# Performance work log

Hardware: AMD Instinct MI355X
Metric: run time of the kernel (lower is better)

The kernel has to match this reference:

```python
import jax, jax.numpy as jnp
import numpy as np
import math

B, S, DIM = 2, 2048, 2048
H, KV = 32, 8
HD = DIM // H          # 64
REP = H // KV          # 4
NEG = -1e9


def setup_inputs() -> dict:
    key = jax.random.key(0)
    ks = jax.random.split(key, 8)
    x = jax.random.normal(ks[0], (B, S, DIM), dtype=jnp.float32)
    # RoPE frequencies: theta = 10000^{-2i/d}, angles = pos * theta
    inv_freq = 1.0 / (10000.0 ** (jnp.arange(0, HD, 2, dtype=jnp.float32) / HD))  # [HD/2]
    angles = jnp.arange(S, dtype=jnp.float32)[:, None] * inv_freq[None, :]        # [S, HD/2]
    freqs_cos = jnp.cos(angles)
    freqs_sin = jnp.sin(angles)
    # additive causal mask [1,1,S,S]
    causal = jnp.tril(jnp.ones((S, S), dtype=bool))
    mask = jnp.where(causal, 0.0, NEG).astype(jnp.float32)[None, None]
    sc = 1.0 / math.sqrt(DIM)
    wq = jax.random.normal(ks[1], (DIM, H * HD), dtype=jnp.float32) * sc
    wk = jax.random.normal(ks[2], (DIM, KV * HD), dtype=jnp.float32) * sc
    wv = jax.random.normal(ks[3], (DIM, KV * HD), dtype=jnp.float32) * sc
    wo = jax.random.normal(ks[4], (H * HD, DIM), dtype=jnp.float32) * sc
    return {"x": x, "freqs_cos": freqs_cos, "freqs_sin": freqs_sin,
            "mask": mask, "wq": wq, "wk": wk, "wv": wv, "wo": wo}


def _rope(t, cos, sin):
    # t: [B,S,nh,HD]; interleaved (even, odd) pairs == view_as_complex layout
    te, to = t[..., 0::2], t[..., 1::2]
    c = cos[None, :, None, :]  # [1,S,1,HD/2]
    s = sin[None, :, None, :]
    oe = te * c - to * s
    oo = te * s + to * c
    return jnp.stack([oe, oo], axis=-1).reshape(t.shape)


def reference(x, freqs_cos, freqs_sin, mask, wq, wk, wv, wo):
    b, s, _ = x.shape
    q = (x @ wq).reshape(b, s, H, HD)
    k = (x @ wk).reshape(b, s, KV, HD)
    v = (x @ wv).reshape(b, s, KV, HD)
    q = _rope(q, freqs_cos, freqs_sin)
    k = _rope(k, freqs_cos, freqs_sin)
    # GQA without materializing repeat_interleave: group q heads by kv head
    # repeat_interleave maps query head h -> kv head h // REP
    qg = q.transpose(0, 2, 1, 3).reshape(b, KV, REP, s, HD)  # [B,KV,REP,S,HD]
    kg = k.transpose(0, 2, 1, 3)                              # [B,KV,S,HD]
    vg = v.transpose(0, 2, 1, 3)
    scores = jnp.einsum('bgrqd,bgkd->bgrqk', qg, kg) / math.sqrt(HD)
    scores = scores + mask[:, :, None]                        # [1,1,1,S,S] broadcast
    attn = jax.nn.softmax(scores, axis=-1)
    out = jnp.einsum('bgrqk,bgkd->bgrqd', attn, vg)           # [B,KV,REP,S,HD]
    out = out.reshape(b, H, s, HD).transpose(0, 2, 1, 3).reshape(b, s, H * HD)
    return out @ wo
```

## Files before the change

### kernel.cpp

```cpp
#include <hip/hip_runtime.h>
#include <hip/hip_bf16.h>

#define B_ 2
#define S_ 2048
#define DIM_ 2048
#define H_ 32
#define KV_ 8
#define HD_ 64

typedef __bf16 bf16x8 __attribute__((ext_vector_type(8)));
typedef __bf16 bf16x4 __attribute__((ext_vector_type(4)));
typedef float f32x4 __attribute__((ext_vector_type(4)));
typedef float f32x16 __attribute__((ext_vector_type(16)));
typedef unsigned u32x2 __attribute__((ext_vector_type(2)));

#define GLOAD16(gp, lp) __builtin_amdgcn_global_load_lds( \
    (const __attribute__((address_space(1))) void*)(gp),  \
    (__attribute__((address_space(3))) void*)(lp), 16, 0, 0)

__global__ __launch_bounds__(256) void cast_f32_bf16_v4(const float* __restrict__ in,
                                                        __bf16* __restrict__ out, int n4) {
    int i = blockIdx.x * 256 + threadIdx.x;
    if (i >= n4) return;
    float4 v = ((const float4*)in)[i];
    bf16x4 o;
    o[0] = (__bf16)v.x; o[1] = (__bf16)v.y; o[2] = (__bf16)v.z; o[3] = (__bf16)v.w;
    ((bf16x4*)out)[i] = o;
}

__global__ __launch_bounds__(256) void transpose_all_t(const float* __restrict__ wq,
                                                       const float* __restrict__ wk,
                                                       const float* __restrict__ wv,
                                                       const float* __restrict__ wo,
                                                       __bf16* __restrict__ wqkv_t,
                                                       __bf16* __restrict__ wo_t) {
    __shared__ float t[32][33];
    const int bk = blockIdx.x * 32, bn = blockIdx.y * 32;
    const int tx = threadIdx.x & 31, ty = threadIdx.x >> 5;
    const float* W; __bf16* Wt; int N, src;
    if (blockIdx.z == 0) {
        Wt = wqkv_t;
        if (bn < 2048)      { W = wq; N = 2048; src = bn; }
        else if (bn < 2560) { W = wk; N = 512;  src = bn - 2048; }
        else                { W = wv; N = 512;  src = bn - 2560; }
    } else {
        if (bn >= 2048) return;
        Wt = wo_t; W = wo; N = 2048; src = bn;
    }
#pragma unroll
    for (int i = 0; i < 4; i++)
        t[ty * 4 + i][tx] = W[(size_t)(bk + ty * 4 + i) * N + src + tx];
    __syncthreads();
#pragma unroll
    for (int i = 0; i < 4; i++)
        Wt[(size_t)(bn + ty * 4 + i) * 2048 + bk + tx] = (__bf16)t[tx][ty * 4 + i];
}

__global__ __launch_bounds__(512, 2)
void gemm256_qkv(const __bf16* __restrict__ A, const __bf16* __restrict__ Bt,
                 __bf16* __restrict__ q_bf, __bf16* __restrict__ k_bf,
                 __bf16* __restrict__ vt_bf,
                 const float* __restrict__ fc, const float* __restrict__ fs) {
    __shared__ __align__(16) char smem[131072];
    char* lA = smem;
    char* lB = smem + 65536;
    const int K = DIM_;
    const int tid = threadIdx.x, lane = tid & 63, wid = tid >> 6;
    const int wr2 = wid >> 2, wc2 = wid & 3;
    const int fr = lane & 15, fg = lane >> 4;
    const long i0 = (long)blockIdx.x * 256;
    const long j0 = (long)blockIdx.y * 256;

    const int r0 = tid >> 3;
    const int cc = ((tid & 7) ^ (r0 & 7)) * 8;
    const __bf16* pA = A + (i0 + r0) * (long)K + cc;
    const __bf16* pB = Bt + (j0 + r0) * (long)K + cc;
    const int NT = K >> 6;

    f32x4 acc[8][4] = {};

#define STGA(h, kt, buf) do { \
    GLOAD16(pA + (long)((h) * 128) * K + (kt) * 64,      lA + (buf) * 32768 + (h) * 16384 + tid * 16); \
    GLOAD16(pA + (long)((h) * 128 + 64) * K + (kt) * 64, lA + (buf) * 32768 + (h) * 16384 + 8192 + tid * 16); } while (0)
#define STGB(h, kt, buf) do { \
    GLOAD16(pB + (long)((h) * 128) * K + (kt) * 64,      lB + (buf) * 32768 + (h) * 16384 + tid * 16); \
    GLOAD16(pB + (long)((h) * 128 + 64) * K + (kt) * 64, lB + (buf) * 32768 + (h) * 16384 + 8192 + tid * 16); } while (0)

    STGA(0, 0, 0); STGB(0, 0, 0); STGB(1, 0, 0); STGA(1, 0, 0);

    for (int kt = 0; kt < NT; ++kt) {
        const int cur = kt & 1, nxt = cur ^ 1;
        const bool nl = (kt + 1 < NT);
        const char* cA = lA + cur * 32768;
        const char* cB = lB + cur * 32768;
        bf16x8 af[4], bfv[4];

        auto rdA = [&](int mf, int ks) -> bf16x8 {
            int row = wr2 * 128 + mf * 16 + fr;
            return *(const bf16x8*)(cA + row * 128 + (((ks << 2) | fg) ^ (row & 7)) * 16);
        };
        auto rdB = [&](int nf, int ks) -> bf16x8 {
            int row = wc2 * 64 + nf * 16 + fr;
            return *(const bf16x8*)(cB + row * 128 + (((ks << 2) | fg) ^ (row & 7)) * 16);
        };

        if (nl) { STGA(0, kt + 1, nxt); STGB(0, kt + 1, nxt); }
        if (nl) asm volatile("s_waitcnt vmcnt(4)" ::: "memory");
        else    asm volatile("s_waitcnt vmcnt(0)" ::: "memory");
        __builtin_amdgcn_s_barrier();
        asm volatile("" ::: "memory");
#pragma unroll
        for (int nf = 0; nf < 4; nf++) bfv[nf] = rdB(nf, 0);
#pragma unroll
        for (int mf = 0; mf < 4; mf++) af[mf] = rdA(mf, 0);
        __builtin_amdgcn_s_setprio(1);
#pragma unroll
        for (int mf = 0; mf < 4; mf++)
#pragma unroll
            for (int nf = 0; nf < 4; nf++)
                acc[mf][nf] = __builtin_amdgcn_mfma_f32_16x16x32_bf16(af[mf], bfv[nf], acc[mf][nf], 0, 0, 0);
        __builtin_amdgcn_s_setprio(0);
        __builtin_amdgcn_s_barrier();

#pragma unroll
        for (int mf = 0; mf < 4; mf++) af[mf] = rdA(4 + mf, 0);
        if (nl) { STGB(1, kt + 1, nxt); STGA(1, kt + 1, nxt); }
        __builtin_amdgcn_s_barrier();
        __builtin_amdgcn_s_setprio(1);
#pragma unroll
        for (int mf = 0; mf < 4; mf++)
#pragma unroll
            for (int nf = 0; nf < 4; nf++)
                acc[4 + mf][nf] = __builtin_amdgcn_mfma_f32_16x16x32_bf16(af[mf], bfv[nf], acc[4 + mf][nf], 0, 0, 0);
        __builtin_amdgcn_s_setprio(0);
        __builtin_amdgcn_s_barrier();

#pragma unroll
        for (int nf = 0; nf < 4; nf++) bfv[nf] = rdB(nf, 1);
#pragma unroll
        for (int mf = 0; mf < 4; mf++) af[mf] = rdA(mf, 1);
        __builtin_amdgcn_s_barrier();
        __builtin_amdgcn_s_setprio(1);
#pragma unroll
        for (int mf = 0; mf < 4; mf++)
#pragma unroll
            for (int nf = 0; nf < 4; nf++)
                acc[mf][nf] = __builtin_amdgcn_mfma_f32_16x16x32_bf16(af[mf], bfv[nf], acc[mf][nf], 0, 0, 0);
        __builtin_amdgcn_s_setprio(0);
        __builtin_amdgcn_s_barrier();

#pragma unroll
        for (int mf = 0; mf < 4; mf++) af[mf] = rdA(4 + mf, 1);
        __builtin_amdgcn_s_barrier();
        __builtin_amdgcn_s_setprio(1);
#pragma unroll
        for (int mf = 0; mf < 4; mf++)
#pragma unroll
            for (int nf = 0; nf < 4; nf++)
                acc[4 + mf][nf] = __builtin_amdgcn_mfma_f32_16x16x32_bf16(af[mf], bfv[nf], acc[4 + mf][nf], 0, 0, 0);
        __builtin_amdgcn_s_setprio(0);
        __builtin_amdgcn_s_barrier();
    }
#undef STGA
#undef STGB

    const long col0 = j0 + wc2 * 64;
    if (j0 < 2048) {
#pragma unroll
        for (int mf = 0; mf < 8; mf++)
#pragma unroll
            for (int nf = 0; nf < 4; nf++)
#pragma unroll
                for (int j = 0; j < 4; j++) {
                    long row = i0 + wr2 * 128 + mf * 16 + fg * 4 + j;
                    q_bf[row * 2048 + col0 + nf * 16 + fr] = (__bf16)acc[mf][nf][j];
                }
    } else if (j0 < 2560) {
#pragma unroll
        for (int mf = 0; mf < 8; mf++)
#pragma unroll
            for (int nf = 0; nf < 4; nf++) {
                const int kd = (int)(col0 + nf * 16 + fr - 2048);
                const int i_ = (kd & 63) >> 1;
                const float sgn = (fr & 1) ? 1.0f : -1.0f;
#pragma unroll
                for (int j = 0; j < 4; j++) {
                    long row = i0 + wr2 * 128 + mf * 16 + fg * 4 + j;
                    int s = (int)(row & (S_ - 1));
                    float cv = fc[s * 32 + i_], sv = fs[s * 32 + i_];
                    float v = acc[mf][nf][j];
                    float p = __shfl_xor(v, 1, 64);
                    k_bf[row * 512 + kd] = (__bf16)(v * cv + sgn * sv * p);
                }
            }
    } else {
#pragma unroll
        for (int mf = 0; mf < 8; mf++)
#pragma unroll
            for (int nf = 0; nf < 4; nf++) {
                const int vd = (int)(col0 + nf * 16 + fr - 2560);
                long row0 = i0 + wr2 * 128 + mf * 16 + fg * 4;
                int b = (int)(row0 >> 11);
                int s = (int)(row0 & (S_ - 1));
                bf16x4 pk;
#pragma unroll
                for (int j = 0; j < 4; j++) pk[j] = (__bf16)acc[mf][nf][j];
                *(bf16x4*)(vt_bf + ((size_t)(b * KV_ + (vd >> 6)) * HD_ + (vd & 63)) * S_ + s) = pk;
            }
    }
}

__global__ __launch_bounds__(512, 2)
void gemm256_o(const __bf16* __restrict__ A, const __bf16* __restrict__ Bt,
               float* __restrict__ C) {
    __shared__ __align__(16) char smem[98304];
    char* lA = smem;
    char* lB = smem + 32768;
    const int K = DIM_;
    const int tid = threadIdx.x, lane = tid & 63, wid = tid >> 6;
    const int wr2 = wid >> 2, wc2 = wid & 3;
    const int fr = lane & 15, fg = lane >> 4;
    const int id = blockIdx.x;
    const long i0 = (long)(id >> 3) * 128;
    const long j0 = (long)(id & 7) * 256;

    const int r0 = tid >> 3;
    const int cc = ((tid & 7) ^ (r0 & 7)) * 8;
    const __bf16* pA = A + (i0 + r0) * (long)K + cc;
    const __bf16* pB = Bt + (j0 + r0) * (long)K + cc;
    const int NT = K >> 6;

    f32x4 acc[4][4] = {};

#define STG(kt, buf) do { \
    GLOAD16(pA + (long)(kt) * 64,                  lA + (buf) * 16384 + tid * 16); \
    GLOAD16(pA + (long)64 * K + (long)(kt) * 64,   lA + (buf) * 16384 + 8192 + tid * 16); \
    GLOAD16(pB + (long)(kt) * 64,                  lB + (buf) * 32768 + tid * 16); \
    GLOAD16(pB + (long)64 * K + (long)(kt) * 64,   lB + (buf) * 32768 + 8192 + tid * 16); \
    GLOAD16(pB + (long)128 * K + (long)(kt) * 64,  lB + (buf) * 32768 + 16384 + tid * 16); \
    GLOAD16(pB + (long)192 * K + (long)(kt) * 64,  lB + (buf) * 32768 + 24576 + tid * 16); } while (0)

    STG(0, 0);

    for (int kt = 0; kt < NT; ++kt) {
        const int cur = kt & 1, nxt = cur ^ 1;
        const bool nl = (kt + 1 < NT);
        const char* cA = lA + cur * 16384;
        const char* cB = lB + cur * 32768;

        if (nl) STG(kt + 1, nxt);
        if (nl) asm volatile("s_waitcnt vmcnt(6)" ::: "memory");
        else    asm volatile("s_waitcnt vmcnt(0)" ::: "memory");
        __builtin_amdgcn_s_barrier();
        asm volatile("" ::: "memory");

        bf16x8 af[4], bfv[4];
#pragma unroll
        for (int ks = 0; ks < 2; ks++) {
#pragma unroll
            for (int nf = 0; nf < 4; nf++) {
                int row = wc2 * 64 + nf * 16 + fr;
                bfv[nf] = *(const bf16x8*)(cB + row * 128 + (((ks << 2) | fg) ^ (row & 7)) * 16);
            }
#pragma unroll
            for (int mf = 0; mf < 4; mf++) {
                int row = wr2 * 64 + mf * 16 + fr;
                af[mf] = *(const bf16x8*)(cA + row * 128 + (((ks << 2) | fg) ^ (row & 7)) * 16);
            }
            __builtin_amdgcn_s_setprio(1);
#pragma unroll
            for (int mf = 0; mf < 4; mf++)
#pragma unroll
                for (int nf = 0; nf < 4; nf++)
                    acc[mf][nf] = __builtin_amdgcn_mfma_f32_16x16x32_bf16(af[mf], bfv[nf], acc[mf][nf], 0, 0, 0);
            __builtin_amdgcn_s_setprio(0);
        }
        __builtin_amdgcn_s_barrier();
    }
#undef STG

#pragma unroll
    for (int mf = 0; mf < 4; mf++)
#pragma unroll
        for (int nf = 0; nf < 4; nf++)
#pragma unroll
            for (int j = 0; j < 4; j++) {
                long row = i0 + wr2 * 64 + mf * 16 + fg * 4 + j;
                long col = j0 + wc2 * 64 + nf * 16 + fr;
                C[row * 2048 + col] = acc[mf][nf][j];
            }
}

__global__ __launch_bounds__(256, 4)
void attn_fwd(const __bf16* __restrict__ Q, const __bf16* __restrict__ Kb,
              const __bf16* __restrict__ Vt, __bf16* __restrict__ O,
              const float* __restrict__ fc, const float* __restrict__ fs) {
    extern __shared__ __align__(16) char smem[];
    __bf16* lK  = (__bf16*)smem;
    __bf16* lVt = (__bf16*)(smem + 16384);

    const int tid = threadIdx.x;
    const int lane = tid & 63;
    const int wid = tid >> 6;
    const int ln = lane & 31;
    const int hi = lane >> 5;

    const int id = blockIdx.x;
    const int round = id >> 8;
    const int q4 = (id >> 6) & 3;
    const int inner = id & 63;
    const int g = inner & 7;
    const int hb = inner >> 3;
    const int b = hb & 1;
    const int h = g * 4 + (hb >> 1);
    const int chunk = (round == 0) ? 12 + q4
                    : (round == 1) ? 3 - q4
                    : (round == 2) ? 8 + q4
                    :                7 - q4;
    const int QS = H_ * HD_, KS = KV_ * HD_;
    const float K2 = 0.18033688011112042f;
    const float mK = 8.0f * K2;

    const __bf16* Kbse = Kb + (size_t)(b * S_) * KS + g * HD_;
    const __bf16* Vbse = Vt + (size_t)((b * KV_ + g) * HD_) * S_;

    bf16x8 onesf;
#pragma unroll
    for (int j = 0; j < 8; j++) onesf[j] = (__bf16)1.0f;

    const int c0 = tid, c1 = tid + 256;
    const int kr0 = c0 & 63, kd0 = c0 >> 6;
    const int kr1 = c1 & 63, kd1 = c1 >> 6;
    const __bf16* Ksrc0 = Kbse + (size_t)kr0 * KS + kd0 * 8;
    const __bf16* Ksrc1 = Kbse + (size_t)kr1 * KS + kd1 * 8;
    const __bf16* Vsrc0 = Vbse + (size_t)kr0 * S_ + kd0 * 8;
    const __bf16* Vsrc1 = Vbse + (size_t)kr1 * S_ + kd1 * 8;

    auto stage = [&](int t, int buf) {
        GLOAD16(Ksrc0 + (size_t)t * 64 * KS, lK + buf * 4096 + c0 * 8);
        GLOAD16(Ksrc1 + (size_t)t * 64 * KS, lK + buf * 4096 + c1 * 8);
        GLOAD16(Vsrc0 + t * 64,              lVt + buf * 4096 + c0 * 8);
        GLOAD16(Vsrc1 + t * 64,              lVt + buf * 4096 + c1 * 8);
    };

    const int q0w = chunk * 128 + wid * 32;
    const int qrow = q0w + ln;
    const int nt = 2 * chunk + 2;
    const int nkv_w = (q0w >> 6) + 1;

    const __bf16* Qb = Q + (size_t)(b * S_ + qrow) * QS + h * HD_;
    const float* cz = fc + (size_t)qrow * 32;
    const float* sz = fs + (size_t)qrow * 32;
    bf16x8 qf[4];
#pragma unroll
    for (int kk = 0; kk < 4; kk++) {
        bf16x8 raw = *(const bf16x8*)(Qb + kk * 16 + hi * 8);
#pragma unroll
        for (int p = 0; p < 4; p++) {
            const int i = kk * 8 + hi * 4 + p;
            float cv = cz[i], sv = sz[i];
            float e = (float)raw[2 * p], o = (float)raw[2 * p + 1];
            qf[kk][2 * p]     = (__bf16)(e * cv - o * sv);
            qf[kk][2 * p + 1] = (__bf16)(e * sv + o * cv);
        }
    }

    f32x16 o0 = {}, o1 = {}, o2 = {};

    stage(0, 0);
    __syncthreads();

    for (int t = 0; t < nt; t++) {
        if (t + 1 < nt) stage(t + 1, (t + 1) & 1);
        if (t < nkv_w) {
            const char* lKc = (const char*)(lK + (t & 1) * 4096);
            const char* lVc = (const char*)(lVt + (t & 1) * 4096);
            const int p0 = t * 64;

            f32x16 s0 = {}, s1 = {};
            __builtin_amdgcn_s_setprio(1);
#pragma unroll
            for (int kk = 0; kk < 4; kk++) {
                bf16x8 ka = *(const bf16x8*)(lKc + (kk * 2 + hi) * 1024 + ln * 16);
                s0 = __builtin_amdgcn_mfma_f32_32x32x16_bf16(ka, qf[kk], s0, 0, 0, 0);
            }
#pragma unroll
            for (int kk = 0; kk < 4; kk++) {
                bf16x8 ka = *(const bf16x8*)(lKc + (kk * 2 + hi) * 1024 + (32 + ln) * 16);
                s1 = __builtin_amdgcn_mfma_f32_32x32x16_bf16(ka, qf[kk], s1, 0, 0, 0);
            }
            __builtin_amdgcn_s_setprio(0);

            if (t == nkv_w - 1) {
#pragma unroll
                for (int rr = 0; rr < 16; rr++) {
                    int crow = (rr & 3) + 8 * (rr >> 2) + 4 * hi;
                    if (p0 + crow > qrow)      s0[rr] = -1e30f;
                    if (p0 + 32 + crow > qrow) s1[rr] = -1e30f;
                }
            }

#pragma unroll
            for (int rr = 0; rr < 16; rr++) {
                s0[rr] = exp2f(s0[rr] * K2 - mK);
                s1[rr] = exp2f(s1[rr] * K2 - mK);
            }

            __builtin_amdgcn_s_setprio(1);
#pragma unroll
            for (int c = 0; c < 2; c++) {
                const f32x16& pe = c ? s1 : s0;
                unsigned w[4][2];
#pragma unroll
                for (int gi = 0; gi < 4; gi++)
#pragma unroll
                    for (int p = 0; p < 2; p++) {
                        unsigned short lo = __builtin_bit_cast(unsigned short, (__bf16)pe[4 * gi + 2 * p]);
                        unsigned short hp = __builtin_bit_cast(unsigned short, (__bf16)pe[4 * gi + 2 * p + 1]);
                        w[gi][p] = (unsigned)lo | ((unsigned)hp << 16);
                    }
                unsigned pw0[4], pw1[4];
#pragma unroll
                for (int p = 0; p < 2; p++) {
                    u32x2 ra = __builtin_amdgcn_permlane32_swap(w[0][p], w[1][p], false, false);
                    pw0[p] = ra[0]; pw0[2 + p] = ra[1];
                    u32x2 rb = __builtin_amdgcn_permlane32_swap(w[2][p], w[3][p], false, false);
                    pw1[p] = rb[0]; pw1[2 + p] = rb[1];
                }
                bf16x8 pa0 = __builtin_bit_cast(bf16x8, *(uint4*)pw0);
                bf16x8 pa1 = __builtin_bit_cast(bf16x8, *(uint4*)pw1);
#pragma unroll
                for (int half = 0; half < 2; half++) {
                    const int ks = 2 * c + half;
                    bf16x8 pa = half ? pa1 : pa0;
                    bf16x8 va0 = *(const bf16x8*)(lVc + (ks * 2 + hi) * 1024 + ln * 16);
                    bf16x8 va1 = *(const bf16x8*)(lVc + (ks * 2 + hi) * 1024 + (32 + ln) * 16);
                    o0 = __builtin_amdgcn_mfma_f32_32x32x16_bf16(va0, pa, o0, 0, 0, 0);
                    o1 = __builtin_amdgcn_mfma_f32_32x32x16_bf16(va1, pa, o1, 0, 0, 0);
                    o2 = __builtin_amdgcn_mfma_f32_32x32x16_bf16(onesf, pa, o2, 0, 0, 0);
                }
            }
            __builtin_amdgcn_s_setprio(0);
        }
        __syncthreads();
    }

    const float inv = 1.0f / o2[0];
    __bf16* Oq = O + (size_t)(b * S_ + qrow) * QS + h * HD_;
#pragma unroll
    for (int db = 0; db < 2; db++) {
        const f32x16& oo = db ? o1 : o0;
#pragma unroll
        for (int gi = 0; gi < 4; gi++) {
            bf16x4 pk;
#pragma unroll
            for (int j = 0; j < 4; j++) pk[j] = (__bf16)(oo[4 * gi + j] * inv);
            *(bf16x4*)(Oq + db * 32 + 8 * gi + 4 * hi) = pk;
        }
    }
}

extern "C" void kernel_launch(void* const* d_in, const int* in_sizes, int n_in,
                              void* d_out, int out_size, void* d_ws, size_t ws_size,
                              hipStream_t stream) {
    const float* x  = (const float*)d_in[0];
    const float* fc = (const float*)d_in[1];
    const float* fs = (const float*)d_in[2];
    const float* wq = (const float*)d_in[4];
    const float* wk = (const float*)d_in[5];
    const float* wv = (const float*)d_in[6];
    const float* wo = (const float*)d_in[7];
    float* out = (float*)d_out;

    const size_t N0 = (size_t)B_ * S_ * DIM_;
    const size_t N1 = (size_t)B_ * S_ * H_ * HD_;
    const size_t N2 = (size_t)B_ * S_ * KV_ * HD_;
    const size_t N3 = (size_t)DIM_ * H_ * HD_;
    const size_t N4 = (size_t)DIM_ * KV_ * HD_;

    __bf16* x_bf = (__bf16*)d_ws;
    __bf16* q_bf = x_bf + N0;
    __bf16* k_bf = q_bf + N1;
    __bf16* vt_bf = k_bf + N2;
    __bf16* wqkv_t = vt_bf + N2;
    __bf16* wo_t = wqkv_t + N3 + 2 * N4;
    __bf16* ao_bf = x_bf;

    cast_f32_bf16_v4<<<dim3(N0 / 4 / 256), 256, 0, stream>>>(x, x_bf, (int)(N0 / 4));
    transpose_all_t<<<dim3(64, 96, 2), 256, 0, stream>>>(wq, wk, wv, wo, wqkv_t, wo_t);

    gemm256_qkv<<<dim3(16, 12), 512, 0, stream>>>(x_bf, wqkv_t, q_bf, k_bf, vt_bf, fc, fs);

    attn_fwd<<<dim3(1024), 256, 32768, stream>>>(q_bf, k_bf, vt_bf, ao_bf, fc, fs);

    gemm256_o<<<dim3(256), 512, 0, stream>>>(ao_bf, wo_t, out);
}
```

Measured before the change: 193.6 us.

## Retile QKV GEMM to 256x192 tiles for full-CU grid, relax attention barriers

```diff
diff --git a/kernel.cpp b/kernel.cpp
--- a/kernel.cpp
+++ b/kernel.cpp
@@ -61,15 +61,16 @@
                  __bf16* __restrict__ q_bf, __bf16* __restrict__ k_bf,
                  __bf16* __restrict__ vt_bf,
                  const float* __restrict__ fc, const float* __restrict__ fs) {
-    __shared__ __align__(16) char smem[131072];
+    __shared__ __align__(16) char smem[114688];
     char* lA = smem;
     char* lB = smem + 65536;
     const int K = DIM_;
     const int tid = threadIdx.x, lane = tid & 63, wid = tid >> 6;
     const int wr2 = wid >> 2, wc2 = wid & 3;
     const int fr = lane & 15, fg = lane >> 4;
-    const long i0 = (long)blockIdx.x * 256;
-    const long j0 = (long)blockIdx.y * 256;
+    const int id = blockIdx.x;
+    const long i0 = (long)(id >> 4) * 256;
+    const long j0 = (long)(id & 15) * 192;
 
     const int r0 = tid >> 3;
     const int cc = ((tid & 7) ^ (r0 & 7)) * 8;
@@ -77,129 +78,82 @@
     const __bf16* pB = Bt + (j0 + r0) * (long)K + cc;
     const int NT = K >> 6;
 
-    f32x4 acc[8][4] = {};
-
-#define STGA(h, kt, buf) do { \
-    GLOAD16(pA + (long)((h) * 128) * K + (kt) * 64,      lA + (buf) * 32768 + (h) * 16384 + tid * 16); \
-    GLOAD16(pA + (long)((h) * 128 + 64) * K + (kt) * 64, lA + (buf) * 32768 + (h) * 16384 + 8192 + tid * 16); } while (0)
-#define STGB(h, kt, buf) do { \
-    GLOAD16(pB + (long)((h) * 128) * K + (kt) * 64,      lB + (buf) * 32768 + (h) * 16384 + tid * 16); \
-    GLOAD16(pB + (long)((h) * 128 + 64) * K + (kt) * 64, lB + (buf) * 32768 + (h) * 16384 + 8192 + tid * 16); } while (0)
-
-    STGA(0, 0, 0); STGB(0, 0, 0); STGB(1, 0, 0); STGA(1, 0, 0);
+    f32x4 acc[8][3] = {};
+
+#define STG(kt, buf) do { \
+    GLOAD16(pA + (long)(kt) * 64,                  lA + (buf) * 32768 + tid * 16); \
+    GLOAD16(pA + (long)64 * K + (long)(kt) * 64,   lA + (buf) * 32768 + 8192 + tid * 16); \
+    GLOAD16(pA + (long)128 * K + (long)(kt) * 64,  lA + (buf) * 32768 + 16384 + tid * 16); \
+    GLOAD16(pA + (long)192 * K + (long)(kt) * 64,  lA + (buf) * 32768 + 24576 + tid * 16); \
+    GLOAD16(pB + (long)(kt) * 64,                  lB + (buf) * 24576 + tid * 16); \
+    GLOAD16(pB + (long)64 * K + (long)(kt) * 64,   lB + (buf) * 24576 + 8192 + tid * 16); \
+    GLOAD16(pB + (long)128 * K + (long)(kt) * 64,  lB + (buf) * 24576 + 16384 + tid * 16); } while (0)
+
+    STG(0, 0);
 
     for (int kt = 0; kt < NT; ++kt) {
         const int cur = kt & 1, nxt = cur ^ 1;
         const bool nl = (kt + 1 < NT);
         const char* cA = lA + cur * 32768;
-        const char* cB = lB + cur * 32768;
-        bf16x8 af[4], bfv[4];
-
-        auto rdA = [&](int mf, int ks) -> bf16x8 {
-            int row = wr2 * 128 + mf * 16 + fr;
-            return *(const bf16x8*)(cA + row * 128 + (((ks << 2) | fg) ^ (row & 7)) * 16);
-        };
-        auto rdB = [&](int nf, int ks) -> bf16x8 {
-            int row = wc2 * 64 + nf * 16 + fr;
-            return *(const bf16x8*)(cB + row * 128 + (((ks << 2) | fg) ^ (row & 7)) * 16);
-        };
-
-        if (nl) { STGA(0, kt + 1, nxt); STGB(0, kt + 1, nxt); }
-        if (nl) asm volatile("s_waitcnt vmcnt(4)" ::: "memory");
+        const char* cB = lB + cur * 24576;
+
+        if (nl) STG(kt + 1, nxt);
+        if (nl) asm volatile("s_waitcnt vmcnt(7)" ::: "memory");
         else    asm volatile("s_waitcnt vmcnt(0)" ::: "memory");
         __builtin_amdgcn_s_barrier();
         asm volatile("" ::: "memory");
-#pragma unroll
-        for (int nf = 0; nf < 4; nf++) bfv[nf] = rdB(nf, 0);
-#pragma unroll
-        for (int mf = 0; mf < 4; mf++) af[mf] = rdA(mf, 0);
-        __builtin_amdgcn_s_setprio(1);
-#pragma unroll
-        for (int mf = 0; mf < 4; mf++)
-#pragma unroll
-            for (int nf = 0; nf < 4; nf++)
-                acc[mf][nf] = __builtin_amdgcn_mfma_f32_16x16x32_bf16(af[mf], bfv[nf], acc[mf][nf], 0, 0, 0);
-        __builtin_amdgcn_s_setprio(0);
-        __builtin_amdgcn_s_barrier();
-
-#pragma unroll
-        for (int mf = 0; mf < 4; mf++) af[mf] = rdA(4 + mf, 0);
-        if (nl) { STGB(1, kt + 1, nxt); STGA(1, kt + 1, nxt); }
-        __builtin_amdgcn_s_barrier();
-        __builtin_amdgcn_s_setprio(1);
-#pragma unroll
-        for (int mf = 0; mf < 4; mf++)
-#pragma unroll
-            for (int nf = 0; nf < 4; nf++)
-                acc[4 + mf][nf] = __builtin_amdgcn_mfma_f32_16x16x32_bf16(af[mf], bfv[nf], acc[4 + mf][nf], 0, 0, 0);
-        __builtin_amdgcn_s_setprio(0);
-        __builtin_amdgcn_s_barrier();
-
-#pragma unroll
-        for (int nf = 0; nf < 4; nf++) bfv[nf] = rdB(nf, 1);
-#pragma unroll
-        for (int mf = 0; mf < 4; mf++) af[mf] = rdA(mf, 1);
-        __builtin_amdgcn_s_barrier();
-        __builtin_amdgcn_s_setprio(1);
-#pragma unroll
-        for (int mf = 0; mf < 4; mf++)
-#pragma unroll
-            for (int nf = 0; nf < 4; nf++)
-                acc[mf][nf] = __builtin_amdgcn_mfma_f32_16x16x32_bf16(af[mf], bfv[nf], acc[mf][nf], 0, 0, 0);
-        __builtin_amdgcn_s_setprio(0);
-        __builtin_amdgcn_s_barrier();
-
-#pragma unroll
-        for (int mf = 0; mf < 4; mf++) af[mf] = rdA(4 + mf, 1);
-        __builtin_amdgcn_s_barrier();
-        __builtin_amdgcn_s_setprio(1);
-#pragma unroll
-        for (int mf = 0; mf < 4; mf++)
-#pragma unroll
-            for (int nf = 0; nf < 4; nf++)
-                acc[4 + mf][nf] = __builtin_amdgcn_mfma_f32_16x16x32_bf16(af[mf], bfv[nf], acc[4 + mf][nf], 0, 0, 0);
-        __builtin_amdgcn_s_setprio(0);
-        __builtin_amdgcn_s_barrier();
-    }
-#undef STGA
-#undef STGB
-
-    const long col0 = j0 + wc2 * 64;
-    if (j0 < 2048) {
-#pragma unroll
-        for (int mf = 0; mf < 8; mf++)
-#pragma unroll
-            for (int nf = 0; nf < 4; nf++)
-#pragma unroll
-                for (int j = 0; j < 4; j++) {
-                    long row = i0 + wr2 * 128 + mf * 16 + fg * 4 + j;
-                    q_bf[row * 2048 + col0 + nf * 16 + fr] = (__bf16)acc[mf][nf][j];
-                }
-    } else if (j0 < 2560) {
-#pragma unroll
-        for (int mf = 0; mf < 8; mf++)
-#pragma unroll
-            for (int nf = 0; nf < 4; nf++) {
-                const int kd = (int)(col0 + nf * 16 + fr - 2048);
+
+        bf16x8 af[8], bfv[3];
+#pragma unroll
+        for (int ks = 0; ks < 2; ks++) {
+#pragma unroll
+            for (int nf = 0; nf < 3; nf++) {
+                int row = wc2 * 48 + nf * 16 + fr;
+                bfv[nf] = *(const bf16x8*)(cB + row * 128 + (((ks << 2) | fg) ^ (row & 7)) * 16);
+            }
+#pragma unroll
+            for (int mf = 0; mf < 8; mf++) {
+                int row = wr2 * 128 + mf * 16 + fr;
+                af[mf] = *(const bf16x8*)(cA + row * 128 + (((ks << 2) | fg) ^ (row & 7)) * 16);
+            }
+            __builtin_amdgcn_s_setprio(1);
+#pragma unroll
+            for (int mf = 0; mf < 8; mf++)
+#pragma unroll
+                for (int nf = 0; nf < 3; nf++)
+                    acc[mf][nf] = __builtin_amdgcn_mfma_f32_16x16x32_bf16(af[mf], bfv[nf], acc[mf][nf], 0, 0, 0);
+            __builtin_amdgcn_s_setprio(0);
+        }
+        __builtin_amdgcn_s_barrier();
+    }
+#undef STG
+
+#pragma unroll
+    for (int mf = 0; mf < 8; mf++)
+#pragma unroll
+        for (int nf = 0; nf < 3; nf++) {
+            const long colf = j0 + wc2 * 48 + nf * 16;
+            const long col = colf + fr;
+            const long row0 = i0 + wr2 * 128 + mf * 16 + fg * 4;
+            if (colf < 2048) {
+#pragma unroll
+                for (int j = 0; j < 4; j++)
+                    q_bf[(row0 + j) * 2048 + col] = (__bf16)acc[mf][nf][j];
+            } else if (colf < 2560) {
+                const int kd = (int)(col - 2048);
                 const int i_ = (kd & 63) >> 1;
                 const float sgn = (fr & 1) ? 1.0f : -1.0f;
 #pragma unroll
                 for (int j = 0; j < 4; j++) {
-                    long row = i0 + wr2 * 128 + mf * 16 + fg * 4 + j;
+                    long row = row0 + j;
                     int s = (int)(row & (S_ - 1));
                     float cv = fc[s * 32 + i_], sv = fs[s * 32 + i_];
                     float v = acc[mf][nf][j];
                     float p = __shfl_xor(v, 1, 64);
                     k_bf[row * 512 + kd] = (__bf16)(v * cv + sgn * sv * p);
                 }
-            }
-    } else {
-#pragma unroll
-        for (int mf = 0; mf < 8; mf++)
-#pragma unroll
-            for (int nf = 0; nf < 4; nf++) {
-                const int vd = (int)(col0 + nf * 16 + fr - 2560);
-                long row0 = i0 + wr2 * 128 + mf * 16 + fg * 4;
+            } else {
+                const int vd = (int)(col - 2560);
                 int b = (int)(row0 >> 11);
                 int s = (int)(row0 & (S_ - 1));
                 bf16x4 pk;
@@ -207,7 +161,7 @@
                 for (int j = 0; j < 4; j++) pk[j] = (__bf16)acc[mf][nf][j];
                 *(bf16x4*)(vt_bf + ((size_t)(b * KV_ + (vd >> 6)) * HD_ + (vd & 63)) * S_ + s) = pk;
             }
-    }
+        }
 }
 
 __global__ __launch_bounds__(512, 2)
@@ -368,10 +322,16 @@
     f32x16 o0 = {}, o1 = {}, o2 = {};
 
     stage(0, 0);
-    __syncthreads();
 
     for (int t = 0; t < nt; t++) {
-        if (t + 1 < nt) stage(t + 1, (t + 1) & 1);
+        if (t + 1 < nt) {
+            stage(t + 1, (t + 1) & 1);
+            asm volatile("s_waitcnt vmcnt(4)" ::: "memory");
+        } else {
+            asm volatile("s_waitcnt vmcnt(0)" ::: "memory");
+        }
+        __builtin_amdgcn_s_barrier();
+        asm volatile("" ::: "memory");
         if (t < nkv_w) {
             const char* lKc = (const char*)(lK + (t & 1) * 4096);
             const char* lVc = (const char*)(lVt + (t & 1) * 4096);
@@ -442,7 +402,7 @@
             }
             __builtin_amdgcn_s_setprio(0);
         }
-        __syncthreads();
+        __builtin_amdgcn_s_barrier();
     }
 
     const float inv = 1.0f / o2[0];
@@ -489,7 +449,7 @@
     cast_f32_bf16_v4<<<dim3(N0 / 4 / 256), 256, 0, stream>>>(x, x_bf, (int)(N0 / 4));
     transpose_all_t<<<dim3(64, 96, 2), 256, 0, stream>>>(wq, wk, wv, wo, wqkv_t, wo_t);
 
-    gemm256_qkv<<<dim3(16, 12), 512, 0, stream>>>(x_bf, wqkv_t, q_bf, k_bf, vt_bf, fc, fs);
+    gemm256_qkv<<<dim3(256), 512, 0, stream>>>(x_bf, wqkv_t, q_bf, k_bf, vt_bf, fc, fs);
 
     attn_fwd<<<dim3(1024), 256, 32768, stream>>>(q_bf, k_bf, vt_bf, ao_bf, fc, fs);
 
```

New measurement: 190.8 us. About the same (-1.5%).
